# Kernel optimization log

Measured on AMD Instinct MI355X. Metric: run time of the kernel, lower is better.

Reference implementation:

```python
import jax, jax.numpy as jnp
import numpy as np

TAU = 0.1      # Gumbel-Sinkhorn temperature (module default)
N_ITER = 100   # Sinkhorn iterations (module default)
B, N = 16, 256


def setup_inputs() -> dict:
    key = jax.random.key(0)
    alpha = jax.random.normal(key, (B, N, N), dtype=jnp.float32)
    return {"alpha": alpha}


def _log_sinkhorn(log_alpha, n_iter):
    # Successive row / column normalization in log space.
    # Note: the torch original early-exits once the column sums are within
    # eps=1e-6 of 1; once converged, further iterations are (numerically)
    # identity, so a fixed n_iter loop computes the same result. We use a
    # fixed-length lax.scan, which runs the whole loop on-device with no
    # per-step host sync.
    def step(la, _):
        la = la - jax.nn.logsumexp(la, axis=-1, keepdims=True)  # row normalize
        la = la - jax.nn.logsumexp(la, axis=-2, keepdims=True)  # col normalize
        return la, None

    log_alpha, _ = jax.lax.scan(step, log_alpha, None, length=n_iter)
    return jnp.exp(log_alpha)


def reference(alpha):
    # Training path of GumbelSinkhornPermutation.forward:
    # scale by temperature, then Sinkhorn-normalize to a near doubly-stochastic
    # matrix. (wandb logging side effects omitted.)
    return _log_sinkhorn(alpha / TAU, N_ITER)
```

## Files before the change

### kernel.cpp

```cpp
#include <hip/hip_runtime.h>

#define N_ITER 100

typedef float f32x4 __attribute__((ext_vector_type(4)));
typedef unsigned u32x4 __attribute__((ext_vector_type(4)));

__device__ __forceinline__ unsigned bf16pack(float a, float b) {
  unsigned ua = __float_as_uint(a), ub = __float_as_uint(b);
  ua = (ua + 0x7FFFu + ((ua >> 16) & 1u)) >> 16;
  ub = (ub + 0x7FFFu + ((ub >> 16) & 1u)) >> 16;
  return ua | (ub << 16);
}
__device__ __forceinline__ float bflo(unsigned u) { return __uint_as_float(u << 16); }
__device__ __forceinline__ float bfhi(unsigned u) { return __uint_as_float(u & 0xFFFF0000u); }

__device__ __forceinline__ void pin_agpr(u32x4& x) {
  asm("" : "=a"(x) : "0"(x));
}

__device__ __forceinline__ void mfma_first(f32x4& acc, const u32x4& a, const u32x4& b) {
  asm("s_nop 2\n\tv_mfma_f32_16x16x32_bf16 %0, %1, %2, 0"
      : "=&a"(acc) : "a"(a), "v"(b));
}
__device__ __forceinline__ void mfma_aa(f32x4& acc, const u32x4& a, const u32x4& b) {
  asm("s_nop 2\n\tv_mfma_f32_16x16x32_bf16 %0, %1, %2, %0"
      : "+a"(acc) : "a"(a), "v"(b));
}
__device__ __forceinline__ void mfma_fence(f32x4& acc0, f32x4& acc1) {
  asm volatile("s_nop 7\n\ts_nop 7\n\ts_nop 7" : "+a"(acc0), "+a"(acc1));
}

__global__ __launch_bounds__(512)
__attribute__((amdgpu_waves_per_eu(2, 2)))
void sinkhorn_mfma8c(const float* __restrict__ alpha, float* __restrict__ out) {
  __shared__ alignas(16) unsigned short Cb16[256];
  __shared__ alignas(16) unsigned short Rb16[256];
  __shared__ alignas(16) float Cb32[256];
  __shared__ alignas(16) float Rb32[256];

  const int tid  = threadIdx.x;
  const int lane = tid & 63;
  const int w    = tid >> 6;
  const int m    = lane & 15;
  const int q    = lane >> 4;

  const size_t mbase = (size_t)blockIdx.x * (256 * 256);
  const float* A = alpha + mbase;
  float*       O = out + mbase;

  u32x4 arow[2][8];
  u32x4 acol[2][8];

#pragma unroll
  for (int s = 0; s < 2; ++s) {
    const float* rowp = A + (size_t)(32 * w + 16 * s + m) * 256 + 8 * q;
#pragma unroll
    for (int c = 0; c < 8; ++c) {
      float4 x0 = *(const float4*)(rowp + 32 * c);
      float4 x1 = *(const float4*)(rowp + 32 * c + 4);
      arow[s][c] = (u32x4){bf16pack(__expf(x0.x * 10.0f), __expf(x0.y * 10.0f)),
                           bf16pack(__expf(x0.z * 10.0f), __expf(x0.w * 10.0f)),
                           bf16pack(__expf(x1.x * 10.0f), __expf(x1.y * 10.0f)),
                           bf16pack(__expf(x1.z * 10.0f), __expf(x1.w * 10.0f))};
    }
    const float* colp = A + (size_t)(8 * q) * 256 + 32 * w + 16 * s + m;
#pragma unroll
    for (int c = 0; c < 8; ++c) {
      const float* p = colp + (size_t)(32 * c) * 256;
      acol[s][c] =
          (u32x4){bf16pack(__expf(p[0] * 10.0f), __expf(p[256] * 10.0f)),
                  bf16pack(__expf(p[512] * 10.0f), __expf(p[768] * 10.0f)),
                  bf16pack(__expf(p[1024] * 10.0f), __expf(p[1280] * 10.0f)),
                  bf16pack(__expf(p[1536] * 10.0f), __expf(p[1792] * 10.0f))};
    }
  }
#pragma unroll
  for (int s = 0; s < 2; ++s)
#pragma unroll
    for (int c = 0; c < 8; ++c) {
      pin_agpr(arow[s][c]);
      pin_agpr(acol[s][c]);
    }

  if (tid < 256) Cb16[tid] = 0x3F80;
  __syncthreads();

  for (int it = 0; it < N_ITER; ++it) {
    const bool last = (it == N_ITER - 1);

    {
      u32x4 B[8];
#pragma unroll
      for (int c = 0; c < 8; ++c) B[c] = *(const u32x4*)&Cb16[32 * c + 8 * q];
      f32x4 acc0, acc1;
      mfma_first(acc0, arow[0][0], B[0]);
      mfma_first(acc1, arow[1][0], B[0]);
#pragma unroll
      for (int c = 1; c < 8; ++c) {
        mfma_aa(acc0, arow[0][c], B[c]);
        mfma_aa(acc1, arow[1][c], B[c]);
      }
      mfma_fence(acc0, acc1);
      if (m == 0) {
        float r0 = __builtin_amdgcn_rcpf(acc0[0]);
        float r1 = __builtin_amdgcn_rcpf(acc0[1]);
        float r2 = __builtin_amdgcn_rcpf(acc0[2]);
        float r3 = __builtin_amdgcn_rcpf(acc0[3]);
        float r4 = __builtin_amdgcn_rcpf(acc1[0]);
        float r5 = __builtin_amdgcn_rcpf(acc1[1]);
        float r6 = __builtin_amdgcn_rcpf(acc1[2]);
        float r7 = __builtin_amdgcn_rcpf(acc1[3]);
        *(uint2*)&Rb16[32 * w + 4 * q] = make_uint2(bf16pack(r0, r1), bf16pack(r2, r3));
        *(uint2*)&Rb16[32 * w + 16 + 4 * q] = make_uint2(bf16pack(r4, r5), bf16pack(r6, r7));
        if (last) {
          *(float4*)&Rb32[32 * w + 4 * q] = make_float4(r0, r1, r2, r3);
          *(float4*)&Rb32[32 * w + 16 + 4 * q] = make_float4(r4, r5, r6, r7);
        }
      }
    }
    __syncthreads();

    {
      u32x4 B[8];
#pragma unroll
      for (int c = 0; c < 8; ++c) B[c] = *(const u32x4*)&Rb16[32 * c + 8 * q];
      f32x4 acc0, acc1;
      mfma_first(acc0, acol[0][0], B[0]);
      mfma_first(acc1, acol[1][0], B[0]);
#pragma unroll
      for (int c = 1; c < 8; ++c) {
        mfma_aa(acc0, acol[0][c], B[c]);
        mfma_aa(acc1, acol[1][c], B[c]);
      }
      mfma_fence(acc0, acc1);
      if (m == 0) {
        float c0 = __builtin_amdgcn_rcpf(acc0[0]);
        float c1 = __builtin_amdgcn_rcpf(acc0[1]);
        float c2 = __builtin_amdgcn_rcpf(acc0[2]);
        float c3 = __builtin_amdgcn_rcpf(acc0[3]);
        float c4 = __builtin_amdgcn_rcpf(acc1[0]);
        float c5 = __builtin_amdgcn_rcpf(acc1[1]);
        float c6 = __builtin_amdgcn_rcpf(acc1[2]);
        float c7 = __builtin_amdgcn_rcpf(acc1[3]);
        *(uint2*)&Cb16[32 * w + 4 * q] = make_uint2(bf16pack(c0, c1), bf16pack(c2, c3));
        *(uint2*)&Cb16[32 * w + 16 + 4 * q] = make_uint2(bf16pack(c4, c5), bf16pack(c6, c7));
        if (last) {
          *(float4*)&Cb32[32 * w + 4 * q] = make_float4(c0, c1, c2, c3);
          *(float4*)&Cb32[32 * w + 16 + 4 * q] = make_float4(c4, c5, c6, c7);
        }
      }
    }
    __syncthreads();
  }

#pragma unroll
  for (int s = 0; s < 2; ++s) {
    const float Rm = Rb32[32 * w + 16 * s + m];
    float* dst = O + (size_t)(32 * w + 16 * s + m) * 256 + 8 * q;
#pragma unroll
    for (int c = 0; c < 8; ++c) {
      float4 c0 = *(const float4*)&Cb32[32 * c + 8 * q];
      float4 c1 = *(const float4*)&Cb32[32 * c + 8 * q + 4];
      u32x4 pk = arow[s][c];
      float4 o0, o1;
      o0.x = bflo(pk.x) * Rm * c0.x;
      o0.y = bfhi(pk.x) * Rm * c0.y;
      o0.z = bflo(pk.y) * Rm * c0.z;
      o0.w = bfhi(pk.y) * Rm * c0.w;
      o1.x = bflo(pk.z) * Rm * c1.x;
      o1.y = bfhi(pk.z) * Rm * c1.y;
      o1.z = bflo(pk.w) * Rm * c1.z;
      o1.w = bfhi(pk.w) * Rm * c1.w;
      *(float4*)(dst + 32 * c) = o0;
      *(float4*)(dst + 32 * c + 4) = o1;
    }
  }
}

extern "C" void kernel_launch(void* const* d_in, const int* in_sizes, int n_in,
                              void* d_out, int out_size, void* d_ws, size_t ws_size,
                              hipStream_t stream) {
  const float* alpha = (const float*)d_in[0];
  float* out = (float*)d_out;
  sinkhorn_mfma8c<<<dim3(16), dim3(512), 0, stream>>>(alpha, out);
}
```

Before: 171.5 us.

## Add per-block convergence check to exit Sinkhorn iterations early

Tracks the maximum deviation of row sums from one, relative to the previous row scaling, and sets a shared flag when any row exceeds a tolerance. Each block breaks out of the iteration loop once all rows are within the tolerance, then runs a final row/column pass that writes the fp32 scalings. This aims to skip iterations once the matrix is already near doubly stochastic. It adds per-iteration comparison work and a shared flag read, and the tolerance is looser than the original early-exit epsilon, which may change accuracy.

```diff
diff --git a/kernel.cpp b/kernel.cpp
--- a/kernel.cpp
+++ b/kernel.cpp
@@ -1,6 +1,7 @@
 #include <hip/hip_runtime.h>
 
 #define N_ITER 100
+#define CONV_EPS 2e-4f
 
 typedef float f32x4 __attribute__((ext_vector_type(4)));
 typedef unsigned u32x4 __attribute__((ext_vector_type(4)));
@@ -32,11 +33,12 @@
 
 __global__ __launch_bounds__(512)
 __attribute__((amdgpu_waves_per_eu(2, 2)))
-void sinkhorn_mfma8c(const float* __restrict__ alpha, float* __restrict__ out) {
+void sinkhorn_mfma8d(const float* __restrict__ alpha, float* __restrict__ out) {
   __shared__ alignas(16) unsigned short Cb16[256];
   __shared__ alignas(16) unsigned short Rb16[256];
   __shared__ alignas(16) float Cb32[256];
   __shared__ alignas(16) float Rb32[256];
+  __shared__ int nc[2];
 
   const int tid  = threadIdx.x;
   const int lane = tid & 63;
@@ -83,11 +85,14 @@
     }
 
   if (tid < 256) Cb16[tid] = 0x3F80;
+  if (tid == 0) { nc[0] = 0; nc[1] = 0; }
   __syncthreads();
 
-  for (int it = 0; it < N_ITER; ++it) {
-    const bool last = (it == N_ITER - 1);
-
+  float rp0 = 1.0f, rp1 = 1.0f, rp2 = 1.0f, rp3 = 1.0f;
+  float rp4 = 1.0f, rp5 = 1.0f, rp6 = 1.0f, rp7 = 1.0f;
+
+  int it = 0;
+  for (; it < N_ITER - 1; ++it) {
     {
       u32x4 B[8];
 #pragma unroll
@@ -101,21 +106,24 @@
         mfma_aa(acc1, arow[1][c], B[c]);
       }
       mfma_fence(acc0, acc1);
+      if (tid == 0) nc[(it + 1) & 1] = 0;
       if (m == 0) {
-        float r0 = __builtin_amdgcn_rcpf(acc0[0]);
-        float r1 = __builtin_amdgcn_rcpf(acc0[1]);
-        float r2 = __builtin_amdgcn_rcpf(acc0[2]);
-        float r3 = __builtin_amdgcn_rcpf(acc0[3]);
-        float r4 = __builtin_amdgcn_rcpf(acc1[0]);
-        float r5 = __builtin_amdgcn_rcpf(acc1[1]);
-        float r6 = __builtin_amdgcn_rcpf(acc1[2]);
-        float r7 = __builtin_amdgcn_rcpf(acc1[3]);
-        *(uint2*)&Rb16[32 * w + 4 * q] = make_uint2(bf16pack(r0, r1), bf16pack(r2, r3));
-        *(uint2*)&Rb16[32 * w + 16 + 4 * q] = make_uint2(bf16pack(r4, r5), bf16pack(r6, r7));
-        if (last) {
-          *(float4*)&Rb32[32 * w + 4 * q] = make_float4(r0, r1, r2, r3);
-          *(float4*)&Rb32[32 * w + 16 + 4 * q] = make_float4(r4, r5, r6, r7);
-        }
+        float d0 = fmaxf(fabsf(fmaf(acc0[0], rp0, -1.0f)), fabsf(fmaf(acc0[1], rp1, -1.0f)));
+        float d1 = fmaxf(fabsf(fmaf(acc0[2], rp2, -1.0f)), fabsf(fmaf(acc0[3], rp3, -1.0f)));
+        float d2 = fmaxf(fabsf(fmaf(acc1[0], rp4, -1.0f)), fabsf(fmaf(acc1[1], rp5, -1.0f)));
+        float d3 = fmaxf(fabsf(fmaf(acc1[2], rp6, -1.0f)), fabsf(fmaf(acc1[3], rp7, -1.0f)));
+        float dev = fmaxf(fmaxf(d0, d1), fmaxf(d2, d3));
+        if (dev > CONV_EPS) nc[it & 1] = 1;
+        rp0 = __builtin_amdgcn_rcpf(acc0[0]);
+        rp1 = __builtin_amdgcn_rcpf(acc0[1]);
+        rp2 = __builtin_amdgcn_rcpf(acc0[2]);
+        rp3 = __builtin_amdgcn_rcpf(acc0[3]);
+        rp4 = __builtin_amdgcn_rcpf(acc1[0]);
+        rp5 = __builtin_amdgcn_rcpf(acc1[1]);
+        rp6 = __builtin_amdgcn_rcpf(acc1[2]);
+        rp7 = __builtin_amdgcn_rcpf(acc1[3]);
+        *(uint2*)&Rb16[32 * w + 4 * q] = make_uint2(bf16pack(rp0, rp1), bf16pack(rp2, rp3));
+        *(uint2*)&Rb16[32 * w + 16 + 4 * q] = make_uint2(bf16pack(rp4, rp5), bf16pack(rp6, rp7));
       }
     }
     __syncthreads();
@@ -144,14 +152,69 @@
         float c7 = __builtin_amdgcn_rcpf(acc1[3]);
         *(uint2*)&Cb16[32 * w + 4 * q] = make_uint2(bf16pack(c0, c1), bf16pack(c2, c3));
         *(uint2*)&Cb16[32 * w + 16 + 4 * q] = make_uint2(bf16pack(c4, c5), bf16pack(c6, c7));
-        if (last) {
-          *(float4*)&Cb32[32 * w + 4 * q] = make_float4(c0, c1, c2, c3);
-          *(float4*)&Cb32[32 * w + 16 + 4 * q] = make_float4(c4, c5, c6, c7);
-        }
       }
     }
     __syncthreads();
-  }
+
+    if (nc[it & 1] == 0) break;
+  }
+
+  {
+    u32x4 B[8];
+#pragma unroll
+    for (int c = 0; c < 8; ++c) B[c] = *(const u32x4*)&Cb16[32 * c + 8 * q];
+    f32x4 acc0, acc1;
+    mfma_first(acc0, arow[0][0], B[0]);
+    mfma_first(acc1, arow[1][0], B[0]);
+#pragma unroll
+    for (int c = 1; c < 8; ++c) {
+      mfma_aa(acc0, arow[0][c], B[c]);
+      mfma_aa(acc1, arow[1][c], B[c]);
+    }
+    mfma_fence(acc0, acc1);
+    if (m == 0) {
+      float r0 = __builtin_amdgcn_rcpf(acc0[0]);
+      float r1 = __builtin_amdgcn_rcpf(acc0[1]);
+      float r2 = __builtin_amdgcn_rcpf(acc0[2]);
+      float r3 = __builtin_amdgcn_rcpf(acc0[3]);
+      float r4 = __builtin_amdgcn_rcpf(acc1[0]);
+      float r5 = __builtin_amdgcn_rcpf(acc1[1]);
+      float r6 = __builtin_amdgcn_rcpf(acc1[2]);
+      float r7 = __builtin_amdgcn_rcpf(acc1[3]);
+      *(uint2*)&Rb16[32 * w + 4 * q] = make_uint2(bf16pack(r0, r1), bf16pack(r2, r3));
+      *(uint2*)&Rb16[32 * w + 16 + 4 * q] = make_uint2(bf16pack(r4, r5), bf16pack(r6, r7));
+      *(float4*)&Rb32[32 * w + 4 * q] = make_float4(r0, r1, r2, r3);
+      *(float4*)&Rb32[32 * w + 16 + 4 * q] = make_float4(r4, r5, r6, r7);
+    }
+  }
+  __syncthreads();
+  {
+    u32x4 B[8];
+#pragma unroll
+    for (int c = 0; c < 8; ++c) B[c] = *(const u32x4*)&Rb16[32 * c + 8 * q];
+    f32x4 acc0, acc1;
+    mfma_first(acc0, acol[0][0], B[0]);
+    mfma_first(acc1, acol[1][0], B[0]);
+#pragma unroll
+    for (int c = 1; c < 8; ++c) {
+      mfma_aa(acc0, acol[0][c], B[c]);
+      mfma_aa(acc1, acol[1][c], B[c]);
+    }
+    mfma_fence(acc0, acc1);
+    if (m == 0) {
+      float c0 = __builtin_amdgcn_rcpf(acc0[0]);
+      float c1 = __builtin_amdgcn_rcpf(acc0[1]);
+      float c2 = __builtin_amdgcn_rcpf(acc0[2]);
+      float c3 = __builtin_amdgcn_rcpf(acc0[3]);
+      float c4 = __builtin_amdgcn_rcpf(acc1[0]);
+      float c5 = __builtin_amdgcn_rcpf(acc1[1]);
+      float c6 = __builtin_amdgcn_rcpf(acc1[2]);
+      float c7 = __builtin_amdgcn_rcpf(acc1[3]);
+      *(float4*)&Cb32[32 * w + 4 * q] = make_float4(c0, c1, c2, c3);
+      *(float4*)&Cb32[32 * w + 16 + 4 * q] = make_float4(c4, c5, c6, c7);
+    }
+  }
+  __syncthreads();
 
 #pragma unroll
   for (int s = 0; s < 2; ++s) {
@@ -182,5 +245,5 @@
                               hipStream_t stream) {
   const float* alpha = (const float*)d_in[0];
   float* out = (float*)d_out;
-  sinkhorn_mfma8c<<<dim3(16), dim3(512), 0, stream>>>(alpha, out);
-}
+  sinkhorn_mfma8d<<<dim3(16), dim3(512), 0, stream>>>(alpha, out);
+}
```

After: 195.0 us. +13.7%, slower.
